# Performance work log

Measured on AMD Instinct MI355X. Metric: run time of the kernel, lower is better.

The kernel has to match this reference:

```python
import jax, jax.numpy as jnp
import numpy as np

SIZES = [8192, 4096, 8192]


def setup_inputs() -> dict:
    key = jax.random.key(0)
    k1, k2, k3 = jax.random.split(key, 3)
    input_data = jax.random.normal(k1, (SIZES[0],), dtype=jnp.float32)
    W0 = jax.random.normal(k2, (SIZES[0], SIZES[1]), dtype=jnp.float32) * 0.05
    W1 = jax.random.normal(k3, (SIZES[1], SIZES[2]), dtype=jnp.float32) * 0.05
    return {"input_data": input_data, "W0": W0, "W1": W1, "steps": 10}


def reference(input_data, W0, W1, steps):
    Ws = [W0, W1]
    L = len(Ws) + 1  # number of layers

    def step(xs, _):
        # top-down predictions: mu[i] = tanh(x[i+1] @ W[i].T); top layer mu stays 0
        mus = [jnp.tanh(xs[i + 1] @ Ws[i].T) for i in range(L - 1)]
        mus.append(jnp.zeros_like(xs[-1]))
        # residual errors
        es = [x - m for x, m in zip(xs, mus)]
        total_error = sum(jnp.sum(e * e) for e in es)
        # state updates (x[0] is clamped to the input, never updated)
        new_xs = [xs[0]]
        for i in range(1, L):
            grad = jnp.clip(-es[i] + es[i - 1] @ Ws[i - 1], -1.0, 1.0)
            new_xs.append(jnp.tanh(xs[i] + 0.01 * grad))
        return tuple(new_xs), total_error

    xs0 = (input_data,) + tuple(jnp.zeros((W.shape[1],), dtype=input_data.dtype) for W in Ws)
    _, errs = jax.lax.scan(step, xs0, None, length=steps)
    # original returns total_error from the final step
    return errs[-1]
```

## Files before the change

### kernel.cpp

```cpp
#include <hip/hip_runtime.h>

#define D0 8192
#define D1 4096
#define D2 8192
#define NB 512

template <int K, bool ACC, bool ERR>
__global__ __launch_bounds__(256) void fused_gemv(
    const float* __restrict__ W, const float* __restrict__ x,
    const float* __restrict__ c, float* __restrict__ e,
    float* __restrict__ part, int M, float* __restrict__ out) {
  constexpr int F4 = K / 1024;
  const int t = threadIdx.x;
  const int lane = t & 63;

  float4 xr[F4];
#pragma unroll
  for (int i = 0; i < F4; ++i)
    xr[i] = *reinterpret_cast<const float4*>(&x[i * 1024 + t * 4]);

  float4 acc[F4];
#pragma unroll
  for (int i = 0; i < F4; ++i) acc[i] = make_float4(0.f, 0.f, 0.f, 0.f);

  const int rpb = M / NB;
  const int r0 = blockIdx.x * rpb;
  const int r1 = r0 + rpb;
  __shared__ float red[4];
  float errsum = 0.f;

  float4 bufA[F4], bufB[F4];

  auto loadrow = [&](float4* buf, int j) {
    const float* wr = W + (size_t)j * K;
#pragma unroll
    for (int i = 0; i < F4; ++i)
      buf[i] = *reinterpret_cast<const float4*>(&wr[i * 1024 + t * 4]);
  };

  auto process = [&](float4* rw, int j) {
    float dp = 0.f;
#pragma unroll
    for (int i = 0; i < F4; ++i)
      dp += rw[i].x * xr[i].x + rw[i].y * xr[i].y + rw[i].z * xr[i].z +
            rw[i].w * xr[i].w;
#pragma unroll
    for (int off = 32; off; off >>= 1) dp += __shfl_down(dp, off, 64);
    if (lane == 0) red[t >> 6] = dp;
    __syncthreads();
    const float ej = c[j] - tanhf(red[0] + red[1] + red[2] + red[3]);
    __syncthreads();
    if (t == 0) e[j] = ej;
    if constexpr (ERR) errsum += ej * ej;
    if constexpr (ACC) {
#pragma unroll
      for (int i = 0; i < F4; ++i) {
        acc[i].x += ej * rw[i].x;
        acc[i].y += ej * rw[i].y;
        acc[i].z += ej * rw[i].z;
        acc[i].w += ej * rw[i].w;
      }
    }
  };

  loadrow(bufA, r0);
  for (int j = r0; j < r1; j += 2) {
    loadrow(bufB, j + 1);
    process(bufA, j);
    loadrow(bufA, (j + 2 < r1) ? j + 2 : r1 - 1);
    process(bufB, j + 1);
  }

  if constexpr (ACC) {
    float* pp = part + (size_t)blockIdx.x * K;
#pragma unroll
    for (int i = 0; i < F4; ++i)
      *reinterpret_cast<float4*>(&pp[i * 1024 + t * 4]) = acc[i];
  }
  if constexpr (ERR) {
    if (t == 0) atomicAdd(out, errsum);
  }
}

__global__ __launch_bounds__(256) void update_kernel(
    float* __restrict__ x1, const float* __restrict__ e1,
    const float* __restrict__ t1p, float* __restrict__ x2,
    const float* __restrict__ t2p) {
  const int t = threadIdx.x;
  const int cl = t & 63;
  const int pl = t >> 6;
  const int base = blockIdx.x * 64;
  __shared__ float red[4][64];
  float s = 0.f;
  if (base < D1) {
    const float* p = t1p + base + cl;
#pragma unroll 8
    for (int k = pl * 128; k < pl * 128 + 128; ++k) s += p[(size_t)k * D1];
  } else {
    const float* p = t2p + (base - D1) + cl;
#pragma unroll 8
    for (int k = pl * 128; k < pl * 128 + 128; ++k) s += p[(size_t)k * D2];
  }
  red[pl][cl] = s;
  __syncthreads();
  if (pl == 0) {
    const float ts = red[0][cl] + red[1][cl] + red[2][cl] + red[3][cl];
    if (base < D1) {
      const int i = base + cl;
      const float g = fminf(fmaxf(-e1[i] + ts, -1.f), 1.f);
      x1[i] = tanhf(x1[i] + 0.01f * g);
    } else {
      const int i = base - D1 + cl;
      const float g = fminf(fmaxf(-x2[i] + ts, -1.f), 1.f);
      x2[i] = tanhf(x2[i] + 0.01f * g);
    }
  }
}

__global__ __launch_bounds__(256) void init_kernel(float* __restrict__ x1,
                                                   float* __restrict__ x2,
                                                   float* __restrict__ e1,
                                                   float* __restrict__ out) {
  int i = blockIdx.x * 256 + threadIdx.x;
  if (i == 0) out[0] = 0.f;
  if (i < D1) {
    x1[i] = 0.f;
    e1[i] = 0.f;
  }
  if (i < D2) x2[i] = 0.f;
}

__global__ __launch_bounds__(256) void sumsq_kernel(const float* __restrict__ x,
                                                    int n,
                                                    float* __restrict__ out) {
  float s = 0.f;
  for (int i = blockIdx.x * 256 + threadIdx.x; i < n; i += gridDim.x * 256)
    s += x[i] * x[i];
#pragma unroll
  for (int off = 32; off; off >>= 1) s += __shfl_down(s, off, 64);
  if ((threadIdx.x & 63) == 0) atomicAdd(out, s);
}

extern "C" void kernel_launch(void* const* d_in, const int* in_sizes, int n_in,
                              void* d_out, int out_size, void* d_ws,
                              size_t ws_size, hipStream_t stream) {
  const float* x0 = (const float*)d_in[0];
  const float* W0 = (const float*)d_in[1];
  const float* W1 = (const float*)d_in[2];
  float* out = (float*)d_out;

  float* ws = (float*)d_ws;
  float* x1 = ws;
  float* x2 = x1 + D1;
  float* e0 = x2 + D2;
  float* e1 = e0 + D0;
  float* t1p = e1 + D1;
  float* t2p = t1p + (size_t)NB * D1;

  const dim3 B(256);

  init_kernel<<<D0 / 256, B, 0, stream>>>(x1, x2, e1, out);
  fused_gemv<D1, true, false>
      <<<NB, B, 0, stream>>>(W0, x1, x0, e0, t1p, D0, nullptr);
  update_kernel<<<D1 / 64, B, 0, stream>>>(x1, e1, t1p, x2, t2p);

  for (int s = 2; s <= 9; ++s) {
    fused_gemv<D1, true, false>
        <<<NB, B, 0, stream>>>(W0, x1, x0, e0, t1p, D0, nullptr);
    fused_gemv<D2, true, false>
        <<<NB, B, 0, stream>>>(W1, x2, x1, e1, t2p, D1, nullptr);
    update_kernel<<<(D1 + D2) / 64, B, 0, stream>>>(x1, e1, t1p, x2, t2p);
  }

  fused_gemv<D1, false, true>
      <<<NB, B, 0, stream>>>(W0, x1, x0, e0, nullptr, D0, out);
  fused_gemv<D2, false, true>
      <<<NB, B, 0, stream>>>(W1, x2, x1, e1, nullptr, D1, out);
  sumsq_kernel<<<8, B, 0, stream>>>(x2, D2, out);
}
```

Measured before the change: 794.9 us.

## Merge both layer GEMV passes into one launch and batch rows per block

The two per-layer fused GEMV kernels for each step become a single launch with 2*NB blocks, which removes a launch and lets the W0 and W1 passes run concurrently. Blocks grow to 512 threads and each block now processes 4 batches of several rows, double-buffered. This issues more independent loads in flight and cuts the per-row syncthreads and reduction overhead to one barrier per batch. In exchange, register pressure rises (16 float4 buffers) and the fixed 4-batch schedule is static_asserted for these sizes.

```diff
diff --git a/kernel.cpp b/kernel.cpp
--- a/kernel.cpp
+++ b/kernel.cpp
@@ -5,80 +5,151 @@
 #define D2 8192
 #define NB 512
 
-template <int K, bool ACC, bool ERR>
-__global__ __launch_bounds__(256) void fused_gemv(
+template <int K, int M, bool ACC, bool ERR>
+__device__ __forceinline__ void fused_body(
     const float* __restrict__ W, const float* __restrict__ x,
     const float* __restrict__ c, float* __restrict__ e,
-    float* __restrict__ part, int M, float* __restrict__ out) {
-  constexpr int F4 = K / 1024;
+    float* __restrict__ part, int bid, float* __restrict__ out) {
+  constexpr int F4 = K / 2048;
+  constexpr int R = 8 / F4;
+  constexpr int RPB = M / NB;
+  static_assert(RPB / R == 4, "schedule below assumes 4 batches");
+
   const int t = threadIdx.x;
   const int lane = t & 63;
+  const int wave = t >> 6;
+  const int r0 = bid * RPB;
+
+  __shared__ float red[2][R][8];
 
   float4 xr[F4];
 #pragma unroll
   for (int i = 0; i < F4; ++i)
-    xr[i] = *reinterpret_cast<const float4*>(&x[i * 1024 + t * 4]);
+    xr[i] = *reinterpret_cast<const float4*>(&x[i * 2048 + t * 4]);
 
   float4 acc[F4];
 #pragma unroll
   for (int i = 0; i < F4; ++i) acc[i] = make_float4(0.f, 0.f, 0.f, 0.f);
 
-  const int rpb = M / NB;
-  const int r0 = blockIdx.x * rpb;
-  const int r1 = r0 + rpb;
-  __shared__ float red[4];
   float errsum = 0.f;
-
-  float4 bufA[F4], bufB[F4];
-
-  auto loadrow = [&](float4* buf, int j) {
-    const float* wr = W + (size_t)j * K;
+  float4 bufA[8], bufB[8];
+
+  auto load = [&](float4* buf, int b) {
+    const float* wp = W + (size_t)(r0 + b * R) * K;
+#pragma unroll
+    for (int r = 0; r < R; ++r)
+#pragma unroll
+      for (int i = 0; i < F4; ++i)
+        buf[r * F4 + i] = *reinterpret_cast<const float4*>(
+            &wp[(size_t)r * K + i * 2048 + t * 4]);
+  };
+
+  auto proc = [&](float4* buf, int b, int par) {
+    const int j0 = r0 + b * R;
+    float dp[R];
+#pragma unroll
+    for (int r = 0; r < R; ++r) {
+      float s = 0.f;
+#pragma unroll
+      for (int i = 0; i < F4; ++i) {
+        const float4 w = buf[r * F4 + i];
+        s += w.x * xr[i].x + w.y * xr[i].y + w.z * xr[i].z + w.w * xr[i].w;
+      }
+      dp[r] = s;
+    }
+#pragma unroll
+    for (int off = 32; off; off >>= 1) {
+#pragma unroll
+      for (int r = 0; r < R; ++r) dp[r] += __shfl_down(dp[r], off, 64);
+    }
+    if (lane == 0) {
+#pragma unroll
+      for (int r = 0; r < R; ++r) red[par][r][wave] = dp[r];
+    }
+    __syncthreads();
+    float ej[R];
+#pragma unroll
+    for (int r = 0; r < R; ++r) {
+      float s = red[par][r][0];
+#pragma unroll
+      for (int w = 1; w < 8; ++w) s += red[par][r][w];
+      ej[r] = c[j0 + r] - tanhf(s);
+    }
+    if (t == 0) {
+#pragma unroll
+      for (int r = 0; r < R; ++r) e[j0 + r] = ej[r];
+      if constexpr (ERR) {
+#pragma unroll
+        for (int r = 0; r < R; ++r) errsum += ej[r] * ej[r];
+      }
+    }
+    if constexpr (ACC) {
+#pragma unroll
+      for (int r = 0; r < R; ++r)
+#pragma unroll
+        for (int i = 0; i < F4; ++i) {
+          acc[i].x += ej[r] * buf[r * F4 + i].x;
+          acc[i].y += ej[r] * buf[r * F4 + i].y;
+          acc[i].z += ej[r] * buf[r * F4 + i].z;
+          acc[i].w += ej[r] * buf[r * F4 + i].w;
+        }
+    }
+  };
+
+  load(bufA, 0);
+  load(bufB, 1);
+  proc(bufA, 0, 0);
+  load(bufA, 2);
+  proc(bufB, 1, 1);
+  load(bufB, 3);
+  proc(bufA, 2, 0);
+  proc(bufB, 3, 1);
+
+  if constexpr (ACC) {
+    float* pp = part + (size_t)bid * K;
 #pragma unroll
     for (int i = 0; i < F4; ++i)
-      buf[i] = *reinterpret_cast<const float4*>(&wr[i * 1024 + t * 4]);
-  };
-
-  auto process = [&](float4* rw, int j) {
-    float dp = 0.f;
-#pragma unroll
-    for (int i = 0; i < F4; ++i)
-      dp += rw[i].x * xr[i].x + rw[i].y * xr[i].y + rw[i].z * xr[i].z +
-            rw[i].w * xr[i].w;
-#pragma unroll
-    for (int off = 32; off; off >>= 1) dp += __shfl_down(dp, off, 64);
-    if (lane == 0) red[t >> 6] = dp;
-    __syncthreads();
-    const float ej = c[j] - tanhf(red[0] + red[1] + red[2] + red[3]);
-    __syncthreads();
-    if (t == 0) e[j] = ej;
-    if constexpr (ERR) errsum += ej * ej;
-    if constexpr (ACC) {
-#pragma unroll
-      for (int i = 0; i < F4; ++i) {
-        acc[i].x += ej * rw[i].x;
-        acc[i].y += ej * rw[i].y;
-        acc[i].z += ej * rw[i].z;
-        acc[i].w += ej * rw[i].w;
-      }
-    }
-  };
-
-  loadrow(bufA, r0);
-  for (int j = r0; j < r1; j += 2) {
-    loadrow(bufB, j + 1);
-    process(bufA, j);
-    loadrow(bufA, (j + 2 < r1) ? j + 2 : r1 - 1);
-    process(bufB, j + 1);
-  }
-
-  if constexpr (ACC) {
-    float* pp = part + (size_t)blockIdx.x * K;
-#pragma unroll
-    for (int i = 0; i < F4; ++i)
-      *reinterpret_cast<float4*>(&pp[i * 1024 + t * 4]) = acc[i];
+      *reinterpret_cast<float4*>(&pp[i * 2048 + t * 4]) = acc[i];
   }
   if constexpr (ERR) {
     if (t == 0) atomicAdd(out, errsum);
+  }
+}
+
+__global__ __launch_bounds__(512, 4) void pass_w0_kernel(
+    const float* __restrict__ W0_, const float* __restrict__ x1_,
+    const float* __restrict__ x0_, float* __restrict__ e0_,
+    float* __restrict__ t1p_) {
+  fused_body<D1, D0, true, false>(W0_, x1_, x0_, e0_, t1p_, blockIdx.x,
+                                  nullptr);
+}
+
+__global__ __launch_bounds__(512, 4) void step_full_kernel(
+    const float* __restrict__ W0_, const float* __restrict__ W1_,
+    const float* __restrict__ x0_, const float* __restrict__ x1_,
+    const float* __restrict__ x2_, float* __restrict__ e0_,
+    float* __restrict__ e1_, float* __restrict__ t1p_,
+    float* __restrict__ t2p_) {
+  if (blockIdx.x < NB) {
+    fused_body<D1, D0, true, false>(W0_, x1_, x0_, e0_, t1p_, blockIdx.x,
+                                    nullptr);
+  } else {
+    fused_body<D2, D1, true, false>(W1_, x2_, x1_, e1_, t2p_, blockIdx.x - NB,
+                                    nullptr);
+  }
+}
+
+__global__ __launch_bounds__(512, 4) void step_err_kernel(
+    const float* __restrict__ W0_, const float* __restrict__ W1_,
+    const float* __restrict__ x0_, const float* __restrict__ x1_,
+    const float* __restrict__ x2_, float* __restrict__ e0_,
+    float* __restrict__ e1_, float* __restrict__ out) {
+  if (blockIdx.x < NB) {
+    fused_body<D1, D0, false, true>(W0_, x1_, x0_, e0_, nullptr, blockIdx.x,
+                                    out);
+  } else {
+    fused_body<D2, D1, false, true>(W1_, x2_, x1_, e1_, nullptr,
+                                    blockIdx.x - NB, out);
   }
 }
 
@@ -157,24 +228,19 @@
   float* t1p = e1 + D1;
   float* t2p = t1p + (size_t)NB * D1;
 
-  const dim3 B(256);
-
-  init_kernel<<<D0 / 256, B, 0, stream>>>(x1, x2, e1, out);
-  fused_gemv<D1, true, false>
-      <<<NB, B, 0, stream>>>(W0, x1, x0, e0, t1p, D0, nullptr);
-  update_kernel<<<D1 / 64, B, 0, stream>>>(x1, e1, t1p, x2, t2p);
+  const dim3 B512(512), B256(256);
+
+  init_kernel<<<D0 / 256, B256, 0, stream>>>(x1, x2, e1, out);
+  pass_w0_kernel<<<NB, B512, 0, stream>>>(W0, x1, x0, e0, t1p);
+  update_kernel<<<D1 / 64, B256, 0, stream>>>(x1, e1, t1p, x2, t2p);
 
   for (int s = 2; s <= 9; ++s) {
-    fused_gemv<D1, true, false>
-        <<<NB, B, 0, stream>>>(W0, x1, x0, e0, t1p, D0, nullptr);
-    fused_gemv<D2, true, false>
-        <<<NB, B, 0, stream>>>(W1, x2, x1, e1, t2p, D1, nullptr);
-    update_kernel<<<(D1 + D2) / 64, B, 0, stream>>>(x1, e1, t1p, x2, t2p);
-  }
-
-  fused_gemv<D1, false, true>
-      <<<NB, B, 0, stream>>>(W0, x1, x0, e0, nullptr, D0, out);
-  fused_gemv<D2, false, true>
-      <<<NB, B, 0, stream>>>(W1, x2, x1, e1, nullptr, D1, out);
-  sumsq_kernel<<<8, B, 0, stream>>>(x2, D2, out);
-}
+    step_full_kernel<<<2 * NB, B512, 0, stream>>>(W0, W1, x0, x1, x2, e0, e1,
+                                                  t1p, t2p);
+    update_kernel<<<(D1 + D2) / 64, B256, 0, stream>>>(x1, e1, t1p, x2, t2p);
+  }
+
+  step_err_kernel<<<2 * NB, B512, 0, stream>>>(W0, W1, x0, x1, x2, e0, e1,
+                                               out);
+  sumsq_kernel<<<8, B256, 0, stream>>>(x2, D2, out);
+}
```

After: 1.087 ms. +36.8%, slower.
